# Optimization experiments

Measured on AMD Instinct MI355X. Metric: run time of the kernel, lower is better.

## Reference

```python
import jax, jax.numpy as jnp
import numpy as np

NUM_HEADS = 8
LN_EPS = 1e-5


def setup_inputs() -> dict:
    key = jax.random.key(0)
    ks = jax.random.split(key, 8)
    B, H, W, C = 2, 64, 64, 256
    return {
        "x": jax.random.normal(ks[0], (B, H, W, C), dtype=jnp.float32),
        "cond": jax.random.normal(ks[1], (B, C), dtype=jnp.float32),
        "t": jax.random.randint(ks[2], (B,), 0, 100, dtype=jnp.int64),
        "emb_table": jax.random.normal(ks[3], (100, C), dtype=jnp.float32) * 0.02,
        "ada_w": jax.random.normal(ks[4], (C, 2 * C), dtype=jnp.float32) * 0.02,
        "ada_b": jnp.zeros((2 * C,), dtype=jnp.float32),
        "qkv_w": jax.random.normal(ks[5], (C, 3 * C), dtype=jnp.float32) * 0.02,
        "qkv_b": jnp.zeros((3 * C,), dtype=jnp.float32),
        "proj_w": jax.random.normal(ks[6], (C, C), dtype=jnp.float32) * 0.02,
        "proj_b": jnp.zeros((C,), dtype=jnp.float32),
    }


def reference(x, cond, t, emb_table, ada_w, ada_b, qkv_w, qkv_b, proj_w, proj_b):
    B, H, W, C = x.shape
    N = H * W
    h = NUM_HEADS
    d = C // h
    scale = d ** -0.5

    x = x.reshape(B, N, C)

    # AdaLayerNorm (adalayernorm_abs): timestep embedding -> SiLU -> Linear -> scale/shift
    emb = emb_table[t]                                # [B, C]
    ss = jax.nn.silu(emb) @ ada_w + ada_b             # [B, 2C]
    sc, sh = jnp.split(ss, 2, axis=-1)                # each [B, C]
    mu = jnp.mean(x, axis=-1, keepdims=True)
    var = jnp.var(x, axis=-1, keepdims=True)
    xn = (x - mu) * jax.lax.rsqrt(var + LN_EPS)       # LN without affine
    x = xn * (1.0 + sc[:, None, :]) + sh[:, None, :]

    # QKV projection and head split
    qkv = (x @ qkv_w + qkv_b).reshape(B, N, 3, h, d)
    qkv = jnp.transpose(qkv, (2, 0, 3, 1, 4))          # [3, B, h, N, d]
    q, k, v = qkv[0], qkv[1], qkv[2]

    # Manual attention: full [B, h, N, N] scores (matches original module)
    attn = jnp.einsum('bhnd,bhmd->bhnm', q, k) * scale
    attn = jax.nn.softmax(attn, axis=-1)
    out = jnp.einsum('bhnm,bhmd->bhnd', attn, v)       # [B, h, N, d]
    out = jnp.transpose(out, (0, 2, 1, 3)).reshape(B, N, C)

    out = (out.reshape(B, H, W, C) @ proj_w) + proj_b
    return out
```

## Files before the change

### kernel.cpp

```cpp
#include <hip/hip_runtime.h>
#include <hip/hip_bf16.h>
#include <stdint.h>

typedef __attribute__((ext_vector_type(8))) short bfrag;
typedef __attribute__((ext_vector_type(4))) short bfrag4;
typedef __attribute__((ext_vector_type(4))) float f32x4;
typedef __attribute__((ext_vector_type(2))) float f32x2;
typedef __attribute__((ext_vector_type(2))) unsigned int u32x2;

__device__ inline short f2bf(float f) {
  union { float f; uint32_t u; } v; v.f = f;
  uint32_t u = v.u;
  uint32_t r = (u + 0x7fffu + ((u >> 16) & 1u)) >> 16;
  return (short)r;
}

__device__ inline uint32_t pack_bf16(float a, float b) {
  uint32_t ua = __builtin_bit_cast(uint32_t, a) + 0x8000u;
  uint32_t ub = __builtin_bit_cast(uint32_t, b) + 0x8000u;
  return __builtin_amdgcn_perm(ub, ua, 0x07060302);
}

__global__ __launch_bounds__(256) void ada_kernel(
    const float* __restrict__ emb_table, const int* __restrict__ t,
    const float* __restrict__ ada_w, const float* __restrict__ ada_b,
    float* __restrict__ scsh) {
  int b = blockIdx.y;
  int tid = threadIdx.x;
  __shared__ float se[256];
  __shared__ float part[256];
  int tt = t[b];
  float e = emb_table[tt * 256 + tid];
  se[tid] = e / (1.f + __expf(-e));
  __syncthreads();
  int ol = tid & 63, kc = tid >> 6;
  int o = blockIdx.x * 64 + ol;
  float acc = 0.f;
#pragma unroll 8
  for (int k = kc * 64; k < (kc + 1) * 64; ++k) acc += se[k] * ada_w[k * 512 + o];
  part[tid] = acc;
  __syncthreads();
  if (tid < 64) {
    int oo = blockIdx.x * 64 + tid;
    scsh[b * 512 + oo] =
        part[tid] + part[64 + tid] + part[128 + tid] + part[192 + tid] + ada_b[oo];
  }
}

__global__ __launch_bounds__(256) void transpose_w(const float* __restrict__ W,
                                                   short* __restrict__ Wt, int N) {
  __shared__ float tile[64][65];
  int k0 = blockIdx.x * 64, n0 = blockIdx.y * 64;
  int tid = threadIdx.x;
  int r = tid >> 2, c0 = (tid & 3) * 16;
  const float* src = W + (long)(k0 + r) * N + n0 + c0;
#pragma unroll
  for (int j = 0; j < 16; j += 4) {
    float4 v = *(const float4*)(src + j);
    tile[r][c0 + j] = v.x; tile[r][c0 + j + 1] = v.y;
    tile[r][c0 + j + 2] = v.z; tile[r][c0 + j + 3] = v.w;
  }
  __syncthreads();
  int nl = tid >> 2, kc = (tid & 3) * 16;
  short outv[16];
#pragma unroll
  for (int j = 0; j < 16; ++j) outv[j] = f2bf(tile[kc + j][nl]);
  short* dst = Wt + (long)(n0 + nl) * 256 + k0 + kc;
  *(bfrag*)dst = *(bfrag*)&outv[0];
  *(bfrag*)(dst + 8) = *(bfrag*)&outv[8];
}

__global__ __launch_bounds__(256) void ln_kernel(const float* __restrict__ x,
                                                 const float* __restrict__ scsh,
                                                 short* __restrict__ xb) {
  int row = blockIdx.x;
  int b = row >> 12;
  int i = threadIdx.x;
  float v = x[(long)row * 256 + i];
  float s = v, sq = v * v;
#pragma unroll
  for (int off = 32; off > 0; off >>= 1) {
    s += __shfl_down(s, off);
    sq += __shfl_down(sq, off);
  }
  __shared__ float red[8];
  int w = i >> 6;
  if ((i & 63) == 0) { red[w] = s; red[4 + w] = sq; }
  __syncthreads();
  s = red[0] + red[1] + red[2] + red[3];
  sq = red[4] + red[5] + red[6] + red[7];
  float mu = s * (1.f / 256.f);
  float var = sq * (1.f / 256.f) - mu * mu;
  float xn = (v - mu) * rsqrtf(var + 1e-5f);
  float y = xn * (1.f + scsh[b * 512 + i]) + scsh[b * 512 + 256 + i];
  xb[(long)row * 256 + i] = f2bf(y);
}

__global__ __launch_bounds__(256) void gemm_bf16(const short* __restrict__ A,
                                                 const short* __restrict__ Bt,
                                                 const float* __restrict__ bias,
                                                 void* __restrict__ Cout, int N,
                                                 int c_fp32, float qscale, int qcols) {
  __shared__ short As[64 * 40];
  __shared__ short Bs[64 * 40];
  const int mt = blockIdx.x, nt = blockIdx.y;
  const int tid = threadIdx.x;
  const int w = tid >> 6, lane = tid & 63, l16 = lane & 15, quad = lane >> 4;
  const int si = tid >> 2, sk = (tid & 3) * 8;
  f32x4 acc[4] = {{0,0,0,0},{0,0,0,0},{0,0,0,0},{0,0,0,0}};
  const short* Arow = A + (long)(mt * 64 + si) * 256 + sk;
  const short* Brow = Bt + (long)(nt * 64 + si) * 256 + sk;
  for (int kk = 0; kk < 8; ++kk) {
    __syncthreads();
    *(bfrag*)&As[si * 40 + sk] = *(const bfrag*)(Arow + kk * 32);
    *(bfrag*)&Bs[si * 40 + sk] = *(const bfrag*)(Brow + kk * 32);
    __syncthreads();
    bfrag a = *(const bfrag*)&As[(w * 16 + l16) * 40 + quad * 8];
#pragma unroll
    for (int c = 0; c < 4; ++c) {
      bfrag bf = *(const bfrag*)&Bs[(c * 16 + l16) * 40 + quad * 8];
      acc[c] = __builtin_amdgcn_mfma_f32_16x16x32_bf16(a, bf, acc[c], 0, 0, 0);
    }
  }
#pragma unroll
  for (int c = 0; c < 4; ++c) {
    int col = nt * 64 + c * 16 + l16;
    float bv = bias[col];
    float mult = (col < qcols) ? qscale : 1.0f;
#pragma unroll
    for (int r = 0; r < 4; ++r) {
      int row = mt * 64 + w * 16 + quad * 4 + r;
      float val = (acc[c][r] + bv) * mult;
      if (c_fp32) ((float*)Cout)[(long)row * N + col] = val;
      else ((short*)Cout)[(long)row * N + col] = f2bf(val);
    }
  }
}

__global__ __launch_bounds__(256) void attn_kernel(const short* __restrict__ qkv,
                                                   short* __restrict__ attn_out) {
  const int blk = blockIdx.x;
  const int qt = blk & 63;
  const int bh = blk >> 6;
  const int b = bh >> 3, hh = bh & 7;
  const int tid = threadIdx.x;
  const int w = tid >> 6, lane = tid & 63, l16 = lane & 15, quad = lane >> 4;

  __shared__ short Ks[2][64 * 40];
  __shared__ short Vt[2][32 * 68];

  const long rowbase = (long)b * 4096;
  const int qrow = qt * 64 + w * 16 + l16;
  bfrag qf = *(const bfrag*)&qkv[(rowbase + qrow) * 768 + hh * 32 + quad * 8];

  f32x4 o0 = {0,0,0,0}, o1 = {0,0,0,0};
  float l_run = 0.f;

  const int si = tid >> 2;
  const int sk = (tid & 3) * 8;
  const short* kbase = qkv + rowbase * 768 + 256 + hh * 32;
  const short* vbase = qkv + rowbase * 768 + 512 + hh * 32;

  bfrag k8 = *(const bfrag*)&kbase[(long)si * 768 + sk];
  bfrag v8 = *(const bfrag*)&vbase[(long)si * 768 + sk];

  int buf = 0;
  for (int kt = 0; kt < 64; ++kt) {
    *(bfrag*)&Ks[buf][si * 40 + sk] = k8;
#pragma unroll
    for (int j = 0; j < 8; ++j) Vt[buf][(sk + j) * 68 + si] = v8[j];
    int ktn = (kt < 63) ? (kt + 1) : 63;
    k8 = *(const bfrag*)&kbase[(long)(ktn * 64 + si) * 768 + sk];
    v8 = *(const bfrag*)&vbase[(long)(ktn * 64 + si) * 768 + sk];
    __syncthreads();

    f32x4 s[4];
#pragma unroll
    for (int nt = 0; nt < 4; ++nt) {
      bfrag kf = *(const bfrag*)&Ks[buf][(nt * 16 + l16) * 40 + quad * 8];
      f32x4 z = {0,0,0,0};
      s[nt] = __builtin_amdgcn_mfma_f32_16x16x32_bf16(kf, qf, z, 0, 0, 0);
    }
    f32x2 rs2 = {0.f, 0.f};
    bfrag4 pb[4];
#pragma unroll
    for (int nt = 0; nt < 4; ++nt) {
      float p0 = __builtin_amdgcn_exp2f(s[nt][0]);
      float p1 = __builtin_amdgcn_exp2f(s[nt][1]);
      float p2 = __builtin_amdgcn_exp2f(s[nt][2]);
      float p3 = __builtin_amdgcn_exp2f(s[nt][3]);
      f32x2 a = {p0, p1}, c = {p2, p3};
      rs2 += a;
      rs2 += c;
      u32x2 packed;
      packed.x = pack_bf16(p0, p1);
      packed.y = pack_bf16(p2, p3);
      pb[nt] = __builtin_bit_cast(bfrag4, packed);
    }
    float rs = rs2.x + rs2.y;
    rs += __shfl_xor(rs, 16);
    rs += __shfl_xor(rs, 32);
    l_run += rs;

#pragma unroll
    for (int nt = 0; nt < 4; ++nt) {
      bfrag4 va = *(const bfrag4*)&Vt[buf][l16 * 68 + nt * 16 + quad * 4];
      o0 = __builtin_amdgcn_mfma_f32_16x16x16bf16_1k(va, pb[nt], o0, 0, 0, 0);
      bfrag4 vb = *(const bfrag4*)&Vt[buf][(16 + l16) * 68 + nt * 16 + quad * 4];
      o1 = __builtin_amdgcn_mfma_f32_16x16x16bf16_1k(vb, pb[nt], o1, 0, 0, 0);
    }
    buf ^= 1;
  }
  float inv = 1.f / l_run;
  long obase = (rowbase + qt * 64 + w * 16 + l16) * 256 + hh * 32;
#pragma unroll
  for (int h = 0; h < 2; ++h) {
    f32x4 oo = h ? o1 : o0;
#pragma unroll
    for (int r2 = 0; r2 < 2; ++r2) {
      *(uint32_t*)&attn_out[obase + h * 16 + quad * 4 + 2 * r2] =
          pack_bf16(oo[2 * r2] * inv, oo[2 * r2 + 1] * inv);
    }
  }
}

extern "C" void kernel_launch(void* const* d_in, const int* in_sizes, int n_in,
                              void* d_out, int out_size, void* d_ws, size_t ws_size,
                              hipStream_t stream) {
  const float* x      = (const float*)d_in[0];
  const int*   t      = (const int*)d_in[2];
  const float* emb    = (const float*)d_in[3];
  const float* ada_w  = (const float*)d_in[4];
  const float* ada_b  = (const float*)d_in[5];
  const float* qkv_w  = (const float*)d_in[6];
  const float* qkv_b  = (const float*)d_in[7];
  const float* proj_w = (const float*)d_in[8];
  const float* proj_b = (const float*)d_in[9];

  char* ws = (char*)d_ws;
  float* scsh     = (float*)(ws);
  short* qkv_wt   = (short*)(ws + 4096);
  short* proj_wt  = (short*)(ws + 397312);
  short* xb       = (short*)(ws + 528384);
  short* qkv_out  = (short*)(ws + 4722688);
  short* attn_out = (short*)(ws + 17305600);

  const float QS = 0.17677669529663687f * 1.4426950408889634f;

  ada_kernel<<<dim3(8, 2), 256, 0, stream>>>(emb, t, ada_w, ada_b, scsh);
  transpose_w<<<dim3(4, 12), 256, 0, stream>>>(qkv_w, qkv_wt, 768);
  transpose_w<<<dim3(4, 4), 256, 0, stream>>>(proj_w, proj_wt, 256);
  ln_kernel<<<8192, 256, 0, stream>>>(x, scsh, xb);
  gemm_bf16<<<dim3(128, 12), 256, 0, stream>>>(xb, qkv_wt, qkv_b, qkv_out, 768, 0, QS, 256);
  attn_kernel<<<1024, 256, 0, stream>>>(qkv_out, attn_out);
  gemm_bf16<<<dim3(128, 4), 256, 0, stream>>>(attn_out, proj_wt, proj_b, d_out, 256, 1, 1.0f, 0);
}
```

Before: 184.9 us.

## Write V pre-transposed from QKV GEMM and process two query tiles per warp

The QKV GEMM epilogue now writes Q/K into a 512-wide buffer and V in a per-head transposed [b,h,d,N] layout. The attention kernel can then load V tiles with vectorized 16-byte stores instead of scattered per-element LDS transposes. Each warp now handles 32 query rows instead of 16, halving the grid to 512 blocks and reusing each K/V LDS tile for twice the MFMA work. The cost is more registers per thread and fewer blocks to fill the GPU.

Measured after the change: 182.4 us. About the same (-1.4%).

```diff
diff --git a/kernel.cpp b/kernel.cpp
--- a/kernel.cpp
+++ b/kernel.cpp
@@ -99,8 +99,10 @@
 __global__ __launch_bounds__(256) void gemm_bf16(const short* __restrict__ A,
                                                  const short* __restrict__ Bt,
                                                  const float* __restrict__ bias,
-                                                 void* __restrict__ Cout, int N,
-                                                 int c_fp32, float qscale, int qcols) {
+                                                 int N, int mode, float qscale,
+                                                 short* __restrict__ qk,
+                                                 short* __restrict__ vT,
+                                                 float* __restrict__ cout) {
   __shared__ short As[64 * 40];
   __shared__ short Bs[64 * 40];
   const int mt = blockIdx.x, nt = blockIdx.y;
@@ -122,26 +124,48 @@
       acc[c] = __builtin_amdgcn_mfma_f32_16x16x32_bf16(a, bf, acc[c], 0, 0, 0);
     }
   }
-#pragma unroll
-  for (int c = 0; c < 4; ++c) {
-    int col = nt * 64 + c * 16 + l16;
-    float bv = bias[col];
-    float mult = (col < qcols) ? qscale : 1.0f;
-#pragma unroll
-    for (int r = 0; r < 4; ++r) {
-      int row = mt * 64 + w * 16 + quad * 4 + r;
-      float val = (acc[c][r] + bv) * mult;
-      if (c_fp32) ((float*)Cout)[(long)row * N + col] = val;
-      else ((short*)Cout)[(long)row * N + col] = f2bf(val);
-    }
-  }
-}
-
-__global__ __launch_bounds__(256) void attn_kernel(const short* __restrict__ qkv,
+  const int row0 = mt * 64 + w * 16 + quad * 4;
+  if (mode == 1) {
+#pragma unroll
+    for (int c = 0; c < 4; ++c) {
+      int col = nt * 64 + c * 16 + l16;
+      float bv = bias[col];
+#pragma unroll
+      for (int r = 0; r < 4; ++r)
+        cout[(long)(row0 + r) * N + col] = acc[c][r] + bv;
+    }
+  } else if (nt < 8) {
+#pragma unroll
+    for (int c = 0; c < 4; ++c) {
+      int col = nt * 64 + c * 16 + l16;
+      float bv = bias[col];
+      float mult = (col < 256) ? qscale : 1.0f;
+#pragma unroll
+      for (int r = 0; r < 4; ++r)
+        qk[(long)(row0 + r) * 512 + col] = f2bf((acc[c][r] + bv) * mult);
+    }
+  } else {
+    const int bb = mt >> 6;
+    const int keyl = row0 & 4095;
+#pragma unroll
+    for (int c = 0; c < 4; ++c) {
+      int col = nt * 64 + c * 16 + l16;
+      float bv = bias[col];
+      int d = col - 512;
+      u32x2 dd;
+      dd.x = pack_bf16(acc[c][0] + bv, acc[c][1] + bv);
+      dd.y = pack_bf16(acc[c][2] + bv, acc[c][3] + bv);
+      *(u32x2*)&vT[((long)(bb * 8 + (d >> 5)) * 32 + (d & 31)) * 4096 + keyl] = dd;
+    }
+  }
+}
+
+__global__ __launch_bounds__(256) void attn_kernel(const short* __restrict__ qk,
+                                                   const short* __restrict__ vT,
                                                    short* __restrict__ attn_out) {
   const int blk = blockIdx.x;
-  const int qt = blk & 63;
-  const int bh = blk >> 6;
+  const int qt = blk & 31;
+  const int bh = blk >> 5;
   const int b = bh >> 3, hh = bh & 7;
   const int tid = threadIdx.x;
   const int w = tid >> 6, lane = tid & 63, l16 = lane & 15, quad = lane >> 4;
@@ -150,76 +174,86 @@
   __shared__ short Vt[2][32 * 68];
 
   const long rowbase = (long)b * 4096;
-  const int qrow = qt * 64 + w * 16 + l16;
-  bfrag qf = *(const bfrag*)&qkv[(rowbase + qrow) * 768 + hh * 32 + quad * 8];
-
-  f32x4 o0 = {0,0,0,0}, o1 = {0,0,0,0};
-  float l_run = 0.f;
-
-  const int si = tid >> 2;
-  const int sk = (tid & 3) * 8;
-  const short* kbase = qkv + rowbase * 768 + 256 + hh * 32;
-  const short* vbase = qkv + rowbase * 768 + 512 + hh * 32;
-
-  bfrag k8 = *(const bfrag*)&kbase[(long)si * 768 + sk];
-  bfrag v8 = *(const bfrag*)&vbase[(long)si * 768 + sk];
+  const int qrow0 = qt * 128 + w * 32 + l16;
+  bfrag qf0 = *(const bfrag*)&qk[(rowbase + qrow0) * 512 + hh * 32 + quad * 8];
+  bfrag qf1 = *(const bfrag*)&qk[(rowbase + qrow0 + 16) * 512 + hh * 32 + quad * 8];
+
+  f32x4 o00 = {0,0,0,0}, o10 = {0,0,0,0};
+  f32x4 o01 = {0,0,0,0}, o11 = {0,0,0,0};
+  f32x2 l0 = {0.f, 0.f}, l1 = {0.f, 0.f};
+
+  const int si = tid >> 2, sk = (tid & 3) * 8;
+  const int vrow = tid >> 3, vcol = (tid & 7) * 8;
+  const short* ksrc = qk + rowbase * 512 + 256 + hh * 32 + (long)si * 512 + sk;
+  const short* vsrc = vT + ((long)bh * 32 + vrow) * 4096 + vcol;
+
+  bfrag k8 = *(const bfrag*)ksrc;
+  bfrag v8 = *(const bfrag*)vsrc;
 
   int buf = 0;
   for (int kt = 0; kt < 64; ++kt) {
     *(bfrag*)&Ks[buf][si * 40 + sk] = k8;
-#pragma unroll
-    for (int j = 0; j < 8; ++j) Vt[buf][(sk + j) * 68 + si] = v8[j];
+    *(bfrag*)&Vt[buf][vrow * 68 + vcol] = v8;
     int ktn = (kt < 63) ? (kt + 1) : 63;
-    k8 = *(const bfrag*)&kbase[(long)(ktn * 64 + si) * 768 + sk];
-    v8 = *(const bfrag*)&vbase[(long)(ktn * 64 + si) * 768 + sk];
+    k8 = *(const bfrag*)(ksrc + (long)ktn * 64 * 512);
+    v8 = *(const bfrag*)(vsrc + ktn * 64);
     __syncthreads();
 
-    f32x4 s[4];
+    f32x4 s0[4], s1[4];
 #pragma unroll
     for (int nt = 0; nt < 4; ++nt) {
       bfrag kf = *(const bfrag*)&Ks[buf][(nt * 16 + l16) * 40 + quad * 8];
       f32x4 z = {0,0,0,0};
-      s[nt] = __builtin_amdgcn_mfma_f32_16x16x32_bf16(kf, qf, z, 0, 0, 0);
-    }
-    f32x2 rs2 = {0.f, 0.f};
-    bfrag4 pb[4];
+      s0[nt] = __builtin_amdgcn_mfma_f32_16x16x32_bf16(kf, qf0, z, 0, 0, 0);
+      s1[nt] = __builtin_amdgcn_mfma_f32_16x16x32_bf16(kf, qf1, z, 0, 0, 0);
+    }
+    bfrag4 pb0[4], pb1[4];
 #pragma unroll
     for (int nt = 0; nt < 4; ++nt) {
-      float p0 = __builtin_amdgcn_exp2f(s[nt][0]);
-      float p1 = __builtin_amdgcn_exp2f(s[nt][1]);
-      float p2 = __builtin_amdgcn_exp2f(s[nt][2]);
-      float p3 = __builtin_amdgcn_exp2f(s[nt][3]);
-      f32x2 a = {p0, p1}, c = {p2, p3};
-      rs2 += a;
-      rs2 += c;
-      u32x2 packed;
-      packed.x = pack_bf16(p0, p1);
-      packed.y = pack_bf16(p2, p3);
-      pb[nt] = __builtin_bit_cast(bfrag4, packed);
-    }
-    float rs = rs2.x + rs2.y;
-    rs += __shfl_xor(rs, 16);
-    rs += __shfl_xor(rs, 32);
-    l_run += rs;
-
+      float a0 = __builtin_amdgcn_exp2f(s0[nt][0]);
+      float a1 = __builtin_amdgcn_exp2f(s0[nt][1]);
+      float a2 = __builtin_amdgcn_exp2f(s0[nt][2]);
+      float a3 = __builtin_amdgcn_exp2f(s0[nt][3]);
+      f32x2 pa = {a0, a1}, pc = {a2, a3};
+      l0 += pa; l0 += pc;
+      u32x2 pk0; pk0.x = pack_bf16(a0, a1); pk0.y = pack_bf16(a2, a3);
+      pb0[nt] = __builtin_bit_cast(bfrag4, pk0);
+      float b0 = __builtin_amdgcn_exp2f(s1[nt][0]);
+      float b1 = __builtin_amdgcn_exp2f(s1[nt][1]);
+      float b2 = __builtin_amdgcn_exp2f(s1[nt][2]);
+      float b3 = __builtin_amdgcn_exp2f(s1[nt][3]);
+      f32x2 pb = {b0, b1}, pd = {b2, b3};
+      l1 += pb; l1 += pd;
+      u32x2 pk1; pk1.x = pack_bf16(b0, b1); pk1.y = pack_bf16(b2, b3);
+      pb1[nt] = __builtin_bit_cast(bfrag4, pk1);
+    }
 #pragma unroll
     for (int nt = 0; nt < 4; ++nt) {
       bfrag4 va = *(const bfrag4*)&Vt[buf][l16 * 68 + nt * 16 + quad * 4];
-      o0 = __builtin_amdgcn_mfma_f32_16x16x16bf16_1k(va, pb[nt], o0, 0, 0, 0);
       bfrag4 vb = *(const bfrag4*)&Vt[buf][(16 + l16) * 68 + nt * 16 + quad * 4];
-      o1 = __builtin_amdgcn_mfma_f32_16x16x16bf16_1k(vb, pb[nt], o1, 0, 0, 0);
+      o00 = __builtin_amdgcn_mfma_f32_16x16x16bf16_1k(va, pb0[nt], o00, 0, 0, 0);
+      o10 = __builtin_amdgcn_mfma_f32_16x16x16bf16_1k(vb, pb0[nt], o10, 0, 0, 0);
+      o01 = __builtin_amdgcn_mfma_f32_16x16x16bf16_1k(va, pb1[nt], o01, 0, 0, 0);
+      o11 = __builtin_amdgcn_mfma_f32_16x16x16bf16_1k(vb, pb1[nt], o11, 0, 0, 0);
     }
     buf ^= 1;
   }
-  float inv = 1.f / l_run;
-  long obase = (rowbase + qt * 64 + w * 16 + l16) * 256 + hh * 32;
+  float ls0 = l0.x + l0.y, ls1 = l1.x + l1.y;
+  ls0 += __shfl_xor(ls0, 16); ls0 += __shfl_xor(ls0, 32);
+  ls1 += __shfl_xor(ls1, 16); ls1 += __shfl_xor(ls1, 32);
+  float inv0 = 1.f / ls0, inv1 = 1.f / ls1;
+  long ob0 = (rowbase + qrow0) * 256 + hh * 32;
+  long ob1 = (rowbase + qrow0 + 16) * 256 + hh * 32;
 #pragma unroll
   for (int h = 0; h < 2; ++h) {
-    f32x4 oo = h ? o1 : o0;
+    f32x4 g0 = h ? o10 : o00;
+    f32x4 g1 = h ? o11 : o01;
 #pragma unroll
     for (int r2 = 0; r2 < 2; ++r2) {
-      *(uint32_t*)&attn_out[obase + h * 16 + quad * 4 + 2 * r2] =
-          pack_bf16(oo[2 * r2] * inv, oo[2 * r2 + 1] * inv);
+      *(uint32_t*)&attn_out[ob0 + h * 16 + quad * 4 + 2 * r2] =
+          pack_bf16(g0[2 * r2] * inv0, g0[2 * r2 + 1] * inv0);
+      *(uint32_t*)&attn_out[ob1 + h * 16 + quad * 4 + 2 * r2] =
+          pack_bf16(g1[2 * r2] * inv1, g1[2 * r2 + 1] * inv1);
     }
   }
 }
@@ -242,7 +276,8 @@
   short* qkv_wt   = (short*)(ws + 4096);
   short* proj_wt  = (short*)(ws + 397312);
   short* xb       = (short*)(ws + 528384);
-  short* qkv_out  = (short*)(ws + 4722688);
+  short* qk_out   = (short*)(ws + 4722688);
+  short* vT       = (short*)(ws + 13111296);
   short* attn_out = (short*)(ws + 17305600);
 
   const float QS = 0.17677669529663687f * 1.4426950408889634f;
@@ -251,7 +286,9 @@
   transpose_w<<<dim3(4, 12), 256, 0, stream>>>(qkv_w, qkv_wt, 768);
   transpose_w<<<dim3(4, 4), 256, 0, stream>>>(proj_w, proj_wt, 256);
   ln_kernel<<<8192, 256, 0, stream>>>(x, scsh, xb);
-  gemm_bf16<<<dim3(128, 12), 256, 0, stream>>>(xb, qkv_wt, qkv_b, qkv_out, 768, 0, QS, 256);
-  attn_kernel<<<1024, 256, 0, stream>>>(qkv_out, attn_out);
-  gemm_bf16<<<dim3(128, 4), 256, 0, stream>>>(attn_out, proj_wt, proj_b, d_out, 256, 1, 1.0f, 0);
-}
+  gemm_bf16<<<dim3(128, 12), 256, 0, stream>>>(xb, qkv_wt, qkv_b, 768, 0, QS,
+                                               qk_out, vT, nullptr);
+  attn_kernel<<<512, 256, 0, stream>>>(qk_out, vT, attn_out);
+  gemm_bf16<<<dim3(128, 4), 256, 0, stream>>>(attn_out, proj_wt, proj_b, 256, 1,
+                                              1.0f, nullptr, nullptr, (float*)d_out);
+}
```
